# Performance work log

Hardware: AMD Instinct MI355X
Metric: run time of the kernel (lower is better)

Reference implementation:

```python
import jax, jax.numpy as jnp
import numpy as np

B, N, F_IN, DEG = 8, 4096, 8, 8
E = B * N * DEG
MAX_RADIUS, NUM_BASIS, HIDDEN = 3.0, 10, 64
MUL0, MUL1 = 32, 16  # irreps_potential = '32x0e + 16x1o'
W_NUMEL = F_IN * (MUL0 + MUL1)  # 384


def setup_inputs() -> dict:
    key = jax.random.key(0)
    k1, k2, k3, k4, k5, k6 = jax.random.split(key, 6)
    node_features = jax.random.normal(k1, (B, N, F_IN), jnp.float32)
    pos = 4.0 * jax.random.uniform(k2, (B, N, 3), dtype=jnp.float32)  # box so many pairs fall inside max_radius
    # static-shape stand-in for radius_graph: DEG random neighbors per node, within each graph, no self loops
    src = jax.random.randint(k3, (B, N * DEG), 0, N)
    off = jax.random.randint(k4, (B, N * DEG), 1, N)
    dst = (src + off) % N
    boff = (jnp.arange(B) * N)[:, None]
    edge_src = (src + boff).reshape(-1).astype(jnp.int32)
    edge_dst = (dst + boff).reshape(-1).astype(jnp.int32)
    W1 = jax.random.normal(k5, (NUM_BASIS, HIDDEN), jnp.float32)
    W2 = jax.random.normal(k6, (HIDDEN, W_NUMEL), jnp.float32)
    return {"node_features": node_features, "pos": pos, "edge_src": edge_src,
            "edge_dst": edge_dst, "W1": W1, "W2": W2}


def _forward(node_features, pos, edge_src, edge_dst, W1, W2):
    pos_flat = pos.reshape(-1, 3)            # [B*N, 3]
    x_flat = node_features.reshape(-1, F_IN)  # [B*N, F_IN]
    edge_vec = pos_flat[edge_src] - pos_flat[edge_dst]  # [E,3]
    r = jnp.sqrt(jnp.sum(edge_vec * edge_vec, axis=1) + 1e-18)  # [E]

    # soft_one_hot_linspace(r, 0, R, num_basis, basis='smooth_finite', cutoff=True) * sqrt(num_basis)
    values = jnp.linspace(0.0, MAX_RADIUS, NUM_BASIS + 2)[1:-1]
    step = values[1] - values[0]
    d = (r[:, None] - values[None, :]) / step
    inside = jnp.abs(d) < 1.0
    y = jnp.where(inside, jnp.maximum(1.0 - d * d, 1e-7), 1.0)
    emb = jnp.where(inside, 1.14136 * jnp.exp(2.0) * jnp.exp(-1.0 / y), 0.0)
    emb = emb * (NUM_BASIS ** 0.5)           # [E, num_basis]

    # soft_unit_step(10 * (1 - r/R))
    t = 10.0 * (1.0 - r / MAX_RADIUS)
    w_cut = jnp.where(t > 0.0, jnp.exp(-1.0 / jnp.where(t > 0.0, t, 1.0)), 0.0)

    # spherical harmonics lmax=2, normalize=True, 'component' normalization
    u = edge_vec / r[:, None]
    ux, uy, uz = u[:, 0], u[:, 1], u[:, 2]
    sh1 = jnp.sqrt(3.0) * u                  # l=1 (component norm); sh0 == 1
    c15 = np.sqrt(15.0)
    sh2 = jnp.stack([c15 * ux * uy, c15 * uy * uz, 0.5 * np.sqrt(5.0) * (3 * uz * uz - 1.0),
                     c15 * ux * uz, 0.5 * c15 * (ux * ux - uy * uy)], axis=1)
    del sh2  # 2e couples 0e input only to 2e, which is absent from '32x0e+16x1o' -> no path

    # FullyConnectedNet([num_basis, hidden, weight_numel], silu) -> per-edge TP weights
    h = jax.nn.silu(emb @ (W1 / np.sqrt(NUM_BASIS)))
    w = h @ (W2 / np.sqrt(HIDDEN))           # [E, 384]
    wA = w[:, : F_IN * MUL0].reshape(-1, F_IN, MUL0)
    wB = w[:, F_IN * MUL0:].reshape(-1, F_IN, MUL1)

    # FullyConnectedTensorProduct (uvw), shared_weights=False, path norm 1/sqrt(fan_in)
    x_src = x_flat[edge_src]                 # gather [E, F_IN]
    inv = 1.0 / np.sqrt(F_IN)
    out0 = jnp.einsum('eu,euw->ew', x_src, wA) * inv            # 0e x 0e -> 32x0e
    out1 = jnp.einsum('eu,ei,euw->ewi', x_src, sh1, wB) * inv   # 0e x 1o -> 16x1o
    potential = jnp.concatenate([out0, out1.reshape(-1, 3 * MUL1)], axis=1)  # [E, 80]

    # scatter-add to destination nodes
    nodes = jax.ops.segment_sum(w_cut[:, None] * potential, edge_dst, num_segments=B * N)
    psi = nodes[:, :3].reshape(B, N, 3)
    curl = jnp.stack([psi[..., 2] - psi[..., 1],
                      psi[..., 0] - psi[..., 2],
                      psi[..., 1] - psi[..., 0]], axis=-1)       # [B, N, 3]
    return curl


def reference(node_features, pos, edge_src, edge_dst, W1, W2):
    return _forward(node_features, pos, edge_src, edge_dst, W1, W2)
```

## Files before the change

### kernel.cpp

```cpp
#include <hip/hip_runtime.h>
#include <hip/hip_fp16.h>


#define THREADS 256
#define RTAB 2048
#define ROWH 64

__global__ __launch_bounds__(THREADS) void se3_build_table(
    const float* __restrict__ W1,
    const float* __restrict__ W2,
    __half* __restrict__ T)
{
    __shared__ float sW1[10 * 65];
    for (int t = threadIdx.x; t < 640; t += THREADS) {
        int j = t >> 6, k = t & 63;
        sW1[j * 65 + k] = W1[t];
    }
    __syncthreads();

    int g = blockIdx.x * THREADS + threadIdx.x;
    if (g >= RTAB * 24) return;
    int i = g / 24;
    int j = g - i * 24;
    int u = j / 3, c = j - u * 3;

    float r = 3.0f * (float)i / (float)(RTAB - 1);

    float psi = 0.0f;
    float t10 = 10.0f - (10.0f / 3.0f) * r;
    if (t10 > 0.0f) {
        const float C0 = 8.43357306907549f;
        float q  = r * (11.0f / 3.0f);
        int   jf = (int)q;
        float da = q - (float)jf;
        float db = da - 1.0f;
        float ya = fmaxf(1.0f - da * da, 1e-7f);
        float yb = fmaxf(1.0f - db * db, 1e-7f);
        int ja = jf - 1, jb = jf;
        float ea = (ja >= 0) ? C0 * __expf(-1.0f / ya) : 0.0f;
        float eb = (jb <= 9) ? C0 * __expf(-1.0f / yb) : 0.0f;
        int jac = ja < 0 ? 0 : ja;
        int jbc = jb > 9 ? 9 : jb;
        const float* w1a = sW1 + jac * 65;
        const float* w1b = sW1 + jbc * 65;
        const float* w2  = W2 + u * 32 + c;

        float acc = 0.0f;
#pragma unroll 8
        for (int k = 0; k < 64; ++k) {
            float pre = ea * w1a[k] + eb * w1b[k];
            float h   = pre * __builtin_amdgcn_rcpf(1.0f + __expf(-pre));
            acc += h * w2[k * 384];
        }
        psi = acc * __expf(-1.0f / t10) * 0.04419417382415922f;
    }

    __half hv = __float2half(psi);
    T[(size_t)i * ROWH + 2 * j] = hv;
    if (i > 0) T[(size_t)(i - 1) * ROWH + 2 * j + 1] = hv;
}

__global__ __launch_bounds__(THREADS) void se3_edge_kernel(
    const float* __restrict__ x,
    const float* __restrict__ pos,
    const int*   __restrict__ esrc,
    const int*   __restrict__ edst,
    const __half* __restrict__ T,
    float*       __restrict__ outbuf,
    int E, int ncopies, int outN)
{
    int e = blockIdx.x * THREADS + threadIdx.x;
    if (e >= E) return;

    int s = esrc[e];
    int d = edst[e];

    float ex = pos[3 * s + 0] - pos[3 * d + 0];
    float ey = pos[3 * s + 1] - pos[3 * d + 1];
    float ez = pos[3 * s + 2] - pos[3 * d + 2];
    float r  = sqrtf(ex * ex + ey * ey + ez * ez + 1e-18f);

    if (r >= 3.0f) return;

    float tq = r * ((float)(RTAB - 1) / 3.0f);
    int   i  = (int)tq;
    if (i > RTAB - 2) i = RTAB - 2;
    float f  = tq - (float)i;

    const float4* rowp = reinterpret_cast<const float4*>(T + (size_t)i * ROWH);
    const float4* xf   = reinterpret_cast<const float4*>(x + 8 * (size_t)s);
    float4 xA = xf[0];
    float4 xB = xf[1];
    float xs[8] = {xA.x, xA.y, xA.z, xA.w, xB.x, xB.y, xB.z, xB.w};

    float p[3] = {0.0f, 0.0f, 0.0f};
#pragma unroll
    for (int qi = 0; qi < 6; ++qi) {
        float4 v = rowp[qi];
        const __half2* h2 = reinterpret_cast<const __half2*>(&v);
#pragma unroll
        for (int m = 0; m < 4; ++m) {
            int j = 4 * qi + m;
            int u = j / 3, c = j - 3 * u;
            float2 ab = __half22float2(h2[m]);
            float val = fmaf(f, ab.y - ab.x, ab.x);
            p[c] = fmaf(xs[u], val, p[c]);
        }
    }

    float* ob = outbuf + (size_t)(blockIdx.x % ncopies) * outN + 3 * d;
    atomicAdd(ob + 0, p[2] - p[1]);
    atomicAdd(ob + 1, p[0] - p[2]);
    atomicAdd(ob + 2, p[1] - p[0]);
}

__global__ __launch_bounds__(THREADS) void se3_reduce_kernel(
    const float* __restrict__ ws, float* __restrict__ out,
    int outN4, int ncopies)
{
    int idx = blockIdx.x * THREADS + threadIdx.x;
    if (idx >= outN4) return;
    const float4* w = reinterpret_cast<const float4*>(ws);
    float4 acc = w[idx];
    for (int c = 1; c < ncopies; ++c) {
        float4 v = w[(size_t)c * outN4 + idx];
        acc.x += v.x; acc.y += v.y; acc.z += v.z; acc.w += v.w;
    }
    reinterpret_cast<float4*>(out)[idx] = acc;
}

extern "C" void kernel_launch(void* const* d_in, const int* in_sizes, int n_in,
                              void* d_out, int out_size, void* d_ws, size_t ws_size,
                              hipStream_t stream) {
    const float* x    = (const float*)d_in[0];
    const float* pos  = (const float*)d_in[1];
    const int*   esrc = (const int*)d_in[2];
    const int*   edst = (const int*)d_in[3];
    const float* W1   = (const float*)d_in[4];
    const float* W2   = (const float*)d_in[5];
    float* out = (float*)d_out;

    int E    = in_sizes[2];
    int outN = out_size;

    size_t tableBytes = (size_t)RTAB * ROWH * sizeof(__half);
    __half* T = (__half*)d_ws;

    int ncopies = 1;
    if (ws_size > tableBytes) {
        size_t rem = ws_size - tableBytes;
        int nc = (int)(rem / ((size_t)outN * sizeof(float)));
        if (nc > 8) nc = 8;
        if (nc < 1) nc = 1;
        ncopies = nc;
    }

    int buildBlocks = (RTAB * 24 + THREADS - 1) / THREADS;
    se3_build_table<<<buildBlocks, THREADS, 0, stream>>>(W1, W2, T);

    int edgeBlocks = (E + THREADS - 1) / THREADS;
    if (ncopies >= 2) {
        float* copies = (float*)((char*)d_ws + tableBytes);
        hipMemsetAsync(copies, 0, (size_t)ncopies * outN * sizeof(float), stream);
        se3_edge_kernel<<<edgeBlocks, THREADS, 0, stream>>>(
            x, pos, esrc, edst, T, copies, E, ncopies, outN);
        int outN4 = outN / 4;
        se3_reduce_kernel<<<(outN4 + THREADS - 1) / THREADS, THREADS, 0, stream>>>(
            copies, out, outN4, ncopies);
    } else {
        hipMemsetAsync(out, 0, (size_t)outN * sizeof(float), stream);
        se3_edge_kernel<<<edgeBlocks, THREADS, 0, stream>>>(
            x, pos, esrc, edst, T, out, E, 1, outN);
    }
}
```

Measured before the change: 105.2 us.

## Fold curl into table, halve atomics, fuse zeroing into table build

The curl components are folded into the lookup table at build time, so each radius row stores two curl channels per input feature instead of three psi components. This halves the table row size and the per-edge loads, and each edge now issues two atomics instead of three because the third component is recovered in the reduce as the negative sum of the other two. Zeroing of the accumulation copies moves into the table-build kernel, replacing the separate memset, and the edge kernel uses unsafeAtomicAdd. The reduce now always runs and writes strided output, and W2 is staged in shared memory during the build.

```diff
diff --git a/kernel.cpp b/kernel.cpp
--- a/kernel.cpp
+++ b/kernel.cpp
@@ -4,29 +4,42 @@
 
 #define THREADS 256
 #define RTAB 2048
-#define ROWH 64
+#define ROWH 32
 
 __global__ __launch_bounds__(THREADS) void se3_build_table(
     const float* __restrict__ W1,
     const float* __restrict__ W2,
-    __half* __restrict__ T)
+    __half* __restrict__ T,
+    float4* __restrict__ zbuf,
+    int zcount4)
 {
     __shared__ float sW1[10 * 65];
+    __shared__ float sW2[64][25];
+
     for (int t = threadIdx.x; t < 640; t += THREADS) {
         int j = t >> 6, k = t & 63;
         sW1[j * 65 + k] = W1[t];
     }
+    for (int t = threadIdx.x; t < 64 * 24; t += THREADS) {
+        int k = t / 24, j = t - 24 * k;
+        int u = j / 3, c = j - 3 * u;
+        sW2[k][j] = W2[k * 384 + u * 32 + c];
+    }
+
+    int g = blockIdx.x * THREADS + threadIdx.x;
+
+    float4 z = make_float4(0.f, 0.f, 0.f, 0.f);
+    for (int idx = g; idx < zcount4; idx += gridDim.x * THREADS)
+        zbuf[idx] = z;
+
     __syncthreads();
 
-    int g = blockIdx.x * THREADS + threadIdx.x;
-    if (g >= RTAB * 24) return;
-    int i = g / 24;
-    int j = g - i * 24;
-    int u = j / 3, c = j - u * 3;
+    if (g >= RTAB * 8) return;
+    int i = g >> 3;
+    int u = g & 7;
 
     float r = 3.0f * (float)i / (float)(RTAB - 1);
-
-    float psi = 0.0f;
+    float q0 = 0.f, q1 = 0.f;
     float t10 = 10.0f - (10.0f / 3.0f) * r;
     if (t10 > 0.0f) {
         const float C0 = 8.43357306907549f;
@@ -43,21 +56,34 @@
         int jbc = jb > 9 ? 9 : jb;
         const float* w1a = sW1 + jac * 65;
         const float* w1b = sW1 + jbc * 65;
-        const float* w2  = W2 + u * 32 + c;
-
-        float acc = 0.0f;
+
+        float a0 = 0.f, a1 = 0.f, a2 = 0.f;
 #pragma unroll 8
         for (int k = 0; k < 64; ++k) {
             float pre = ea * w1a[k] + eb * w1b[k];
             float h   = pre * __builtin_amdgcn_rcpf(1.0f + __expf(-pre));
-            acc += h * w2[k * 384];
+            a0 = fmaf(h, sW2[k][u * 3 + 0], a0);
+            a1 = fmaf(h, sW2[k][u * 3 + 1], a1);
+            a2 = fmaf(h, sW2[k][u * 3 + 2], a2);
         }
-        psi = acc * __expf(-1.0f / t10) * 0.04419417382415922f;
-    }
-
-    __half hv = __float2half(psi);
-    T[(size_t)i * ROWH + 2 * j] = hv;
-    if (i > 0) T[(size_t)(i - 1) * ROWH + 2 * j + 1] = hv;
+        float sc = __expf(-1.0f / t10) * 0.04419417382415922f;
+        q0 = (a2 - a1) * sc;
+        q1 = (a0 - a2) * sc;
+    }
+
+    __half h0 = __float2half(q0);
+    __half h1 = __float2half(q1);
+    size_t base = (size_t)i * ROWH + 4 * u;
+    T[base + 0] = h0;
+    T[base + 2] = h1;
+    if (i > 0) {
+        T[base - ROWH + 1] = h0;
+        T[base - ROWH + 3] = h1;
+    }
+    if (i == RTAB - 1) {
+        T[base + 1] = h0;
+        T[base + 3] = h1;
+    }
 }
 
 __global__ __launch_bounds__(THREADS) void se3_edge_kernel(
@@ -67,7 +93,7 @@
     const int*   __restrict__ edst,
     const __half* __restrict__ T,
     float*       __restrict__ outbuf,
-    int E, int ncopies, int outN)
+    int E, int ncopies, int outN2)
 {
     int e = blockIdx.x * THREADS + threadIdx.x;
     if (e >= E) return;
@@ -89,44 +115,50 @@
 
     const float4* rowp = reinterpret_cast<const float4*>(T + (size_t)i * ROWH);
     const float4* xf   = reinterpret_cast<const float4*>(x + 8 * (size_t)s);
+    float4 r0 = rowp[0], r1 = rowp[1], r2 = rowp[2], r3 = rowp[3];
     float4 xA = xf[0];
     float4 xB = xf[1];
-    float xs[8] = {xA.x, xA.y, xA.z, xA.w, xB.x, xB.y, xB.z, xB.w};
-
-    float p[3] = {0.0f, 0.0f, 0.0f};
-#pragma unroll
-    for (int qi = 0; qi < 6; ++qi) {
-        float4 v = rowp[qi];
-        const __half2* h2 = reinterpret_cast<const __half2*>(&v);
-#pragma unroll
-        for (int m = 0; m < 4; ++m) {
-            int j = 4 * qi + m;
-            int u = j / 3, c = j - 3 * u;
-            float2 ab = __half22float2(h2[m]);
-            float val = fmaf(f, ab.y - ab.x, ab.x);
-            p[c] = fmaf(xs[u], val, p[c]);
-        }
-    }
-
-    float* ob = outbuf + (size_t)(blockIdx.x % ncopies) * outN + 3 * d;
-    atomicAdd(ob + 0, p[2] - p[1]);
-    atomicAdd(ob + 1, p[0] - p[2]);
-    atomicAdd(ob + 2, p[1] - p[0]);
+    float x0 = xA.x, x1 = xA.y, x2 = xA.z, x3 = xA.w;
+    float x4 = xB.x, x5 = xB.y, x6 = xB.z, x7 = xB.w;
+
+    float c0 = 0.f, c1 = 0.f;
+    auto proc = [&](float4 v, float xu, float xv) {
+        union { float4 f4; __half2 h[4]; } cv; cv.f4 = v;
+        float2 a0 = __half22float2(cv.h[0]);
+        float2 a1 = __half22float2(cv.h[1]);
+        float2 a2 = __half22float2(cv.h[2]);
+        float2 a3 = __half22float2(cv.h[3]);
+        c0 = fmaf(xu, fmaf(f, a0.y - a0.x, a0.x), c0);
+        c1 = fmaf(xu, fmaf(f, a1.y - a1.x, a1.x), c1);
+        c0 = fmaf(xv, fmaf(f, a2.y - a2.x, a2.x), c0);
+        c1 = fmaf(xv, fmaf(f, a3.y - a3.x, a3.x), c1);
+    };
+    proc(r0, x0, x1);
+    proc(r1, x2, x3);
+    proc(r2, x4, x5);
+    proc(r3, x6, x7);
+
+    float* ob = outbuf + (size_t)(blockIdx.x % ncopies) * outN2 + 2 * d;
+    unsafeAtomicAdd(ob + 0, c0);
+    unsafeAtomicAdd(ob + 1, c1);
 }
 
 __global__ __launch_bounds__(THREADS) void se3_reduce_kernel(
     const float* __restrict__ ws, float* __restrict__ out,
-    int outN4, int ncopies)
+    int nNodes, int ncopies, int outN2)
 {
-    int idx = blockIdx.x * THREADS + threadIdx.x;
-    if (idx >= outN4) return;
-    const float4* w = reinterpret_cast<const float4*>(ws);
-    float4 acc = w[idx];
-    for (int c = 1; c < ncopies; ++c) {
-        float4 v = w[(size_t)c * outN4 + idx];
-        acc.x += v.x; acc.y += v.y; acc.z += v.z; acc.w += v.w;
-    }
-    reinterpret_cast<float4*>(out)[idx] = acc;
+    int n = blockIdx.x * THREADS + threadIdx.x;
+    if (n >= nNodes) return;
+    const float2* w = reinterpret_cast<const float2*>(ws);
+    int stride2 = outN2 >> 1;
+    float a = 0.f, b = 0.f;
+    for (int c = 0; c < ncopies; ++c) {
+        float2 v = w[(size_t)c * stride2 + n];
+        a += v.x; b += v.y;
+    }
+    out[3 * n + 0] = a;
+    out[3 * n + 1] = b;
+    out[3 * n + 2] = -a - b;
 }
 
 extern "C" void kernel_launch(void* const* d_in, const int* in_sizes, int n_in,
@@ -140,36 +172,32 @@
     const float* W2   = (const float*)d_in[5];
     float* out = (float*)d_out;
 
-    int E    = in_sizes[2];
-    int outN = out_size;
+    int E      = in_sizes[2];
+    int outN   = out_size;
+    int nNodes = outN / 3;
+    int outN2  = 2 * nNodes;
 
     size_t tableBytes = (size_t)RTAB * ROWH * sizeof(__half);
-    __half* T = (__half*)d_ws;
-
+    __half* T      = (__half*)d_ws;
+    float*  copies = (float*)((char*)d_ws + tableBytes);
+
+    size_t copyBytes = (size_t)outN2 * sizeof(float);
     int ncopies = 1;
-    if (ws_size > tableBytes) {
+    if (ws_size > tableBytes + copyBytes) {
         size_t rem = ws_size - tableBytes;
-        int nc = (int)(rem / ((size_t)outN * sizeof(float)));
+        int nc = (int)(rem / copyBytes);
         if (nc > 8) nc = 8;
         if (nc < 1) nc = 1;
         ncopies = nc;
     }
-
-    int buildBlocks = (RTAB * 24 + THREADS - 1) / THREADS;
-    se3_build_table<<<buildBlocks, THREADS, 0, stream>>>(W1, W2, T);
-
-    int edgeBlocks = (E + THREADS - 1) / THREADS;
-    if (ncopies >= 2) {
-        float* copies = (float*)((char*)d_ws + tableBytes);
-        hipMemsetAsync(copies, 0, (size_t)ncopies * outN * sizeof(float), stream);
-        se3_edge_kernel<<<edgeBlocks, THREADS, 0, stream>>>(
-            x, pos, esrc, edst, T, copies, E, ncopies, outN);
-        int outN4 = outN / 4;
-        se3_reduce_kernel<<<(outN4 + THREADS - 1) / THREADS, THREADS, 0, stream>>>(
-            copies, out, outN4, ncopies);
-    } else {
-        hipMemsetAsync(out, 0, (size_t)outN * sizeof(float), stream);
-        se3_edge_kernel<<<edgeBlocks, THREADS, 0, stream>>>(
-            x, pos, esrc, edst, T, out, E, 1, outN);
-    }
-}
+    int zcount4 = (int)(((size_t)ncopies * outN2) / 4);
+
+    se3_build_table<<<(RTAB * 8) / THREADS, THREADS, 0, stream>>>(
+        W1, W2, T, (float4*)copies, zcount4);
+
+    se3_edge_kernel<<<(E + THREADS - 1) / THREADS, THREADS, 0, stream>>>(
+        x, pos, esrc, edst, T, copies, E, ncopies, outN2);
+
+    se3_reduce_kernel<<<(nNodes + THREADS - 1) / THREADS, THREADS, 0, stream>>>(
+        copies, out, nNodes, ncopies, outN2);
+}
```

Measured after the change: 95.78 us. -8.9%, faster.
